# Performance work log

Measured on AMD Instinct MI355X. Metric: run time of the kernel, lower is better.

Reference implementation:

```python
import jax, jax.numpy as jnp
import numpy as np

P = 30          # points per cloud (nr_points)
K = 20          # knn neighbors (k)
KS = 5          # spline kernel size (control points)
FN = 10         # filter_nr
EPS = 1e-8


def setup_inputs() -> dict:
    key = jax.random.key(0)
    ks = jax.random.split(key, 7)
    B = 16384
    pos = jax.random.normal(ks[0], (B * P, 3), dtype=jnp.float32)
    W = jax.random.normal(ks[1], (KS, FN), dtype=jnp.float32) * 0.5
    b_dsc = jnp.zeros((FN,), dtype=jnp.float32)
    w1 = jax.random.normal(ks[2], (FN, 256), dtype=jnp.float32) * (1.0 / np.sqrt(FN))
    b1 = jnp.zeros((256,), dtype=jnp.float32)
    w2 = jax.random.normal(ks[3], (256, 40), dtype=jnp.float32) * (1.0 / np.sqrt(256.0))
    b2 = jnp.zeros((40,), dtype=jnp.float32)
    return {"pos": pos, "W": W, "b_dsc": b_dsc, "w1": w1, "b1": b1, "w2": w2, "b2": b2}


def _dsc(pos, W, b_dsc):
    # pos: [N,3] -> per-point directional spline conv features [N, FN]
    B = pos.shape[0] // P
    p = pos.reshape(B, P, 3)
    # knn within each cloud (loop=False): pairwise sq dists, mask self
    d2 = jnp.sum((p[:, :, None, :] - p[:, None, :, :]) ** 2, axis=-1)  # [B,P,P]
    d2 = d2 + jnp.eye(P, dtype=d2.dtype) * 1e10
    _, idx = jax.lax.top_k(-d2, K)  # [B,P,K] nearest neighbor indices
    nb = jax.vmap(lambda pts, ii: pts[ii])(p, idx)  # [B,P,K,3] gather
    rel = nb - p[:, :, None, :]                      # [B,P,K,3]
    # normalize neighborhood into unit ball
    norm = jnp.sqrt(jnp.sum(rel * rel, axis=-1) + EPS)      # [B,P,K]
    scale = jnp.max(norm, axis=-1, keepdims=True) + EPS     # [B,P,1]
    rel_n = rel / scale[..., None]
    # dominant local direction via power iteration on 3x3 covariance
    C = jnp.einsum('bpki,bpkj->bpij', rel_n, rel_n)  # [B,P,3,3]
    v = jnp.ones((B, P, 3), dtype=pos.dtype) / jnp.sqrt(3.0)
    for _ in range(8):
        v = jnp.einsum('bpij,bpj->bpi', C, v)
        v = v / (jnp.sqrt(jnp.sum(v * v, axis=-1, keepdims=True)) + EPS)
    # directional coordinate in [-1,1] -> spline parameter in [0, KS-1]
    t = jnp.einsum('bpki,bpi->bpk', rel_n, v)        # [B,P,K]
    u = jnp.clip((t + 1.0) * 0.5, 0.0, 1.0) * (KS - 1)
    i0 = jnp.clip(jnp.floor(u), 0, KS - 2).astype(jnp.int32)  # [B,P,K]
    frac = (u - i0.astype(u.dtype))[..., None]                 # [B,P,K,1]
    feat = W[i0] * (1.0 - frac) + W[i0 + 1] * frac             # [B,P,K,FN]
    y = jnp.mean(feat, axis=2) + b_dsc                         # [B,P,FN]
    return y.reshape(B * P, FN)


def reference(pos, W, b_dsc, w1, b1, w2, b2):
    y = _dsc(pos, W, b_dsc)                  # [N, FN]
    y = jax.nn.sigmoid(y)
    ys = y.reshape(-1, P, FN).mean(axis=1)   # [B, FN]
    h = jax.nn.elu(ys @ w1 + b1)             # [B, 256]
    logits = h @ w2 + b2                     # [B, 40]
    return jax.nn.log_softmax(logits, axis=1)
```

## Files before the change

kernel.cpp:

```cpp
#include <hip/hip_runtime.h>
#include <math.h>

#define NP 30
#define KNN 20
#define KS 5
#define FN 10
#define EPS 1e-8f
#define CPB 16
#define T1 512

typedef __attribute__((ext_vector_type(8))) short short8v;
typedef __attribute__((ext_vector_type(4))) float float4v;

__device__ __forceinline__ float satf(float x) {
    return fminf(fmaxf(x, 0.0f), 1.0f);
}
__device__ __forceinline__ unsigned short bf16r(float f) {
    unsigned u = __float_as_uint(f);
    u += 0x7fffu + ((u >> 16) & 1u);
    return (unsigned short)(u >> 16);
}
__device__ __forceinline__ float rlanef(float v, int l) {
    return __int_as_float(__builtin_amdgcn_readlane(__float_as_int(v), l));
}
__device__ __forceinline__ int hA_idx(int row, int col) {
    return row * 256 + ((((col >> 3) ^ (row & 7)) << 3) | (col & 7));
}
__device__ __forceinline__ float packdi(float v, int j) {
    return __uint_as_float((__float_as_uint(v) & ~31u) | (unsigned)j);
}

__global__ __launch_bounds__(T1, 4) void fused_kernel(
    const float* __restrict__ pos,
    const float* __restrict__ W,
    const float* __restrict__ b_dsc,
    const float* __restrict__ w1,
    const float* __restrict__ b1,
    const float* __restrict__ w2,
    const float* __restrict__ b2,
    float* __restrict__ out,
    int B)
{
    __shared__ float4 ptsF[CPB * NP];
    __shared__ float sb[CPB * NP][11];
    __shared__ __align__(16) float Gs[CPB][12];
    __shared__ float wS[KS * FN];
    __shared__ float bS[FN];
    __shared__ float ysS[CPB * FN];
    __shared__ __align__(16) unsigned short hA[16 * 256];
    __shared__ float Lg[CPB][48];

    const int tid  = threadIdx.x;
    const int base = blockIdx.x * CPB;
    const int w    = tid >> 6;
    const int lane = tid & 63;

    if (tid < CPB * NP) {
        int gp = base * NP + tid;
        if (gp < B * NP) {
            const float* pp = pos + (size_t)gp * 3;
            float x = pp[0], y = pp[1], z = pp[2];
            float n2 = fmaf(z, z, fmaf(y, y, x * x));
            ptsF[tid] = make_float4(x, y, z, n2);
        } else {
            ptsF[tid] = make_float4(0.f, 0.f, 0.f, 0.f);
        }
    }
    if (tid < KS * FN) wS[tid] = W[tid] * (-0.07213475204444817f);
    if (tid < FN)      bS[tid] = b_dsc[tid] * (-1.4426950408889634f);
    __syncthreads();

    const int c = tid / NP;
    const int i = tid - c * NP;
    const bool active = (tid < CPB * NP) && (base + c < B);

    float vals[32];
    float ox = 0.f, oy = 0.f, oz = 0.f, oo = 0.f;

    if (active) {
        const float4* cp = &ptsF[c * NP];
        float4 own = cp[i];
        ox = own.x; oy = own.y; oz = own.z; oo = own.w;

        sb[tid][0] = ox * ox; sb[tid][1] = ox * oy; sb[tid][2] = ox * oz;
        sb[tid][3] = oy * oy; sb[tid][4] = oy * oz; sb[tid][5] = oz * oz;
        sb[tid][6] = ox;      sb[tid][7] = oy;     sb[tid][8] = oz;

        #pragma unroll
        for (int j = 0; j < NP; ++j) {
            float4 q = cp[j];
            float dt = fmaf(q.z, oz, fmaf(q.y, oy, q.x * ox));
            float key = fmaf(-2.0f, dt, q.w);
            vals[j] = packdi(key, j);
            if ((j % 5) == 4) asm volatile("" ::: "memory");
        }
        vals[30] = packdi(1e11f, 30);
        vals[31] = packdi(1e11f, 31);

        #pragma unroll
        for (int k = 2; k <= 16; k <<= 1) {
            #pragma unroll
            for (int jj = k >> 1; jj > 0; jj >>= 1) {
                #pragma unroll
                for (int tt = 0; tt < 32; ++tt) {
                    int l = tt ^ jj;
                    if (l > tt) {
                        float a  = vals[tt], b = vals[l];
                        float lo = fminf(a, b), hi = fmaxf(a, b);
                        if ((tt & k) == 0) { vals[tt] = lo; vals[l] = hi; }
                        else               { vals[tt] = hi; vals[l] = lo; }
                    }
                }
            }
        }
        #pragma unroll
        for (int q = 0; q < 16; ++q) {
            float a = vals[q], b = vals[16 + q];
            vals[q] = fminf(a, b); vals[16 + q] = fmaxf(a, b);
        }
        #pragma unroll
        for (int jj = 8; jj > 0; jj >>= 1) {
            #pragma unroll
            for (int tt = 16; tt < 32; ++tt) {
                int l = tt ^ jj;
                if (l > tt) {
                    float a = vals[tt], b = vals[l];
                    vals[tt] = fminf(a, b); vals[l] = fmaxf(a, b);
                }
            }
        }
    }
    __syncthreads();

    if (tid < CPB * 9) {
        int cc   = tid / 9;
        int comp = tid - cc * 9;
        if (base + cc < B) {
            float s = 0.0f;
            #pragma unroll
            for (int k = 0; k < NP; ++k) s += sb[cc * NP + k][comp];
            Gs[cc][comp] = s;
        }
    }
    __syncthreads();

    if (active) {
        const float4* cp = &ptsF[c * NP];
        const float thr_key = __uint_as_float(__float_as_uint(vals[20]) & ~31u);
        const float thr_d2  = thr_key + oo;
        const float scale   = sqrtf(thr_d2 + EPS) + EPS;
        const float inv_s   = __builtin_amdgcn_rcpf(scale);

        float4 g0 = *(const float4*)&Gs[c][0];
        float4 g1 = *(const float4*)&Gs[c][4];
        float  sx = g1.z, sy = g1.w, sz = Gs[c][8];
        float ax = fmaf(30.f, ox, -sx);
        float ay = fmaf(30.f, oy, -sy);
        float az = fmaf(30.f, oz, -sz);
        float cxx = fmaf(ox, ax, fmaf(-sx, ox, g0.x));
        float cxy = fmaf(oy, ax, fmaf(-sy, ox, g0.y));
        float cxz = fmaf(oz, ax, fmaf(-sz, ox, g0.z));
        float cyy = fmaf(oy, ay, fmaf(-sy, oy, g0.w));
        float cyz = fmaf(oz, ay, fmaf(-sz, oy, g1.x));
        float czz = fmaf(oz, az, fmaf(-sz, oz, g1.y));

        unsigned excl = 0u;
        #pragma unroll
        for (int q2 = 21; q2 < 30; ++q2) {
            unsigned bq  = __float_as_uint(vals[q2]);
            int      idx = (int)(bq & 31u);
            float4 p = cp[idx];
            float dx = p.x - ox, dy = p.y - oy, dz = p.z - oz;
            cxx = fmaf(-dx, dx, cxx); cxy = fmaf(-dx, dy, cxy); cxz = fmaf(-dx, dz, cxz);
            cyy = fmaf(-dy, dy, cyy); cyz = fmaf(-dy, dz, cyz); czz = fmaf(-dz, dz, czz);
            excl |= (1u << idx);
        }

        float tr = cxx + cyy + czz + 1e-30f;
        float rt = __builtin_amdgcn_rcpf(tr);
        float xx = cxx*rt, xy = cxy*rt, xz = cxz*rt;
        float yy = cyy*rt, yz = cyz*rt, zz = czz*rt;
        #pragma unroll
        for (int it = 0; it < 3; ++it) {
            float nxx = fmaf(xx, xx, fmaf(xy, xy, xz * xz));
            float nxy = fmaf(xy, xx + yy, xz * yz);
            float nxz = fmaf(xz, xx + zz, xy * yz);
            float nyy = fmaf(xy, xy, fmaf(yy, yy, yz * yz));
            float nyz = fmaf(yz, yy + zz, xy * xz);
            float nzz = fmaf(xz, xz, fmaf(yz, yz, zz * zz));
            xx = nxx; xy = nxy; xz = nxz; yy = nyy; yz = nyz; zz = nzz;
        }
        float vx = xx + xy + xz;
        float vy = xy + yy + yz;
        float vz = xz + yz + zz;
        float nn = fmaf(vz, vz, fmaf(vy, vy, vx * vx)) + 1e-30f;
        float rr2 = __builtin_amdgcn_rsqf(nn) * inv_s * 2.0f;
        const float wax = vx * rr2, way = vy * rr2, waz = vz * rr2;
        const float c0  = 2.0f - fmaf(oz, waz, fmaf(oy, way, ox * wax));

        float a0 = 0.f, a1 = 0.f, a3 = 0.f, s1 = 0.f;
        #pragma unroll 5
        for (int j = 0; j < NP; ++j) {
            float4 q = cp[j];
            float ur = fmaf(q.z, waz, fmaf(q.y, way, fmaf(q.x, wax, c0)));
            float u  = ((excl >> j) & 1u) ? 2.0f : ur;
            a0 += satf(1.0f - u);
            a1 += satf(1.0f - fabsf(u - 1.0f));
            a3 += satf(1.0f - fabsf(u - 3.0f));
            s1 += u;
        }
        const float P  = 30.0f - a0 - a1 - a3;
        const float Q  = s1 - a1 - 3.0f * a3;
        const float a4 = fmaf(0.5f, Q, -P);
        const float a2 = P - a4 - 10.0f;

        #pragma unroll
        for (int f = 0; f < FN; ++f) {
            float acc = fmaf(a0, wS[0*FN+f],
                        fmaf(a1, wS[1*FN+f],
                        fmaf(a2, wS[2*FN+f],
                        fmaf(a3, wS[3*FN+f],
                             a4 * wS[4*FN+f]))));
            float z2 = acc + bS[f];
            sb[tid][f] = __builtin_amdgcn_rcpf(1.0f + exp2f(z2));
        }
    }
    __syncthreads();

    if (tid < CPB * FN) {
        int c2 = tid / FN;
        float s = 0.0f;
        #pragma unroll
        for (int jj = 0; jj < NP; ++jj) s += sb[c2 * NP + jj][tid - c2 * FN];
        ysS[tid] = (base + c2 < B) ? s * (1.0f / (float)NP) : 0.0f;
    }
    __syncthreads();

    {
        const int  hu    = tid & 255;
        const int  ybase = (w >= 4) ? 80 : 0;
        const int  rbase = (w >= 4) ? 8 : 0;
        float ya = ysS[ybase + lane];
        float yb = ysS[ybase + 64 + (lane & 15)];
        float wv[FN];
        #pragma unroll
        for (int f = 0; f < FN; ++f) wv[f] = w1[f * 256 + hu];
        float bb = b1[hu];
        #pragma unroll
        for (int cc = 0; cc < 8; ++cc) {
            float acc = bb;
            #pragma unroll
            for (int f = 0; f < FN; ++f) {
                const int flat = cc * FN + f;
                float yv = (flat < 64) ? rlanef(ya, flat) : rlanef(yb, flat - 64);
                acc = fmaf(yv, wv[f], acc);
            }
            float h = acc > 0.0f ? acc : __expf(acc) - 1.0f;
            hA[hA_idx(rbase + cc, hu)] = bf16r(h);
        }
    }
    __syncthreads();

    if (w < 3) {
        const int  n   = w * 16 + (lane & 15);
        const bool nok = n < 40;
        const int  kg  = (lane >> 4) * 8;
        float4v acc = {0.f, 0.f, 0.f, 0.f};
        #pragma unroll
        for (int s = 0; s < 8; ++s) {
            short8v bfr;
            #pragma unroll
            for (int j = 0; j < 8; ++j) {
                float f = nok ? w2[(s * 32 + kg + j) * 40 + n] : 0.0f;
                bfr[j] = (short)bf16r(f);
            }
            short8v a = *(const short8v*)&hA[hA_idx(lane & 15, kg + s * 32)];
            acc = __builtin_amdgcn_mfma_f32_16x16x32_bf16(a, bfr, acc, 0, 0, 0);
        }
        if (nok) {
            const float bc = b2[n];
            const int   r0 = (lane >> 4) * 4;
            #pragma unroll
            for (int r = 0; r < 4; ++r) {
                Lg[r0 + r][n] = acc[r] + bc;
            }
        }
    }
    __syncthreads();

    if (tid < CPB * 16) {
        int cl = tid >> 4, l = tid & 15;
        float v0 = Lg[cl][l];
        float v1 = Lg[cl][l + 16];
        float v2 = (l < 8) ? Lg[cl][l + 32] : -INFINITY;
        float m = fmaxf(fmaxf(v0, v1), v2);
        #pragma unroll
        for (int msk = 1; msk < 16; msk <<= 1) m = fmaxf(m, __shfl_xor(m, msk));
        float e = __expf(v0 - m) + __expf(v1 - m) + ((l < 8) ? __expf(v2 - m) : 0.0f);
        #pragma unroll
        for (int msk = 1; msk < 16; msk <<= 1) e += __shfl_xor(e, msk);
        float ls = m + __logf(e);
        int cloud = base + cl;
        if (cloud < B) {
            float* op = out + (size_t)cloud * 40;
            op[l]      = v0 - ls;
            op[16 + l] = v1 - ls;
            if (l < 8) op[32 + l] = v2 - ls;
        }
    }
}

extern "C" void kernel_launch(void* const* d_in, const int* in_sizes, int n_in,
                              void* d_out, int out_size, void* d_ws, size_t ws_size,
                              hipStream_t stream) {
    const float* pos   = (const float*)d_in[0];
    const float* W     = (const float*)d_in[1];
    const float* b_dsc = (const float*)d_in[2];
    const float* w1    = (const float*)d_in[3];
    const float* b1    = (const float*)d_in[4];
    const float* w2    = (const float*)d_in[5];
    const float* b2    = (const float*)d_in[6];

    const int N = in_sizes[0] / 3;
    const int B = N / NP;

    const int grid = (B + CPB - 1) / CPB;
    fused_kernel<<<grid, T1, 0, stream>>>(pos, W, b_dsc, w1, b1, w2, b2,
                                          (float*)d_out, B);
}
```

Measured before the change: 31.56 us.

## Replace full bitonic sort with pruned two-half selection network; read weights directly

```diff
diff --git a/kernel.cpp b/kernel.cpp
--- a/kernel.cpp
+++ b/kernel.cpp
@@ -29,6 +29,9 @@
 __device__ __forceinline__ float packdi(float v, int j) {
     return __uint_as_float((__float_as_uint(v) & ~31u) | (unsigned)j);
 }
+
+#define CEA(A, B) { float a_ = vals[A], b_ = vals[B]; vals[A] = fminf(a_, b_); vals[B] = fmaxf(a_, b_); }
+#define CED(A, B) { float a_ = vals[A], b_ = vals[B]; vals[A] = fmaxf(a_, b_); vals[B] = fminf(a_, b_); }
 
 __global__ __launch_bounds__(T1, 4) void fused_kernel(
     const float* __restrict__ pos,
@@ -44,8 +47,6 @@
     __shared__ float4 ptsF[CPB * NP];
     __shared__ float sb[CPB * NP][11];
     __shared__ __align__(16) float Gs[CPB][12];
-    __shared__ float wS[KS * FN];
-    __shared__ float bS[FN];
     __shared__ float ysS[CPB * FN];
     __shared__ __align__(16) unsigned short hA[16 * 256];
     __shared__ float Lg[CPB][48];
@@ -66,8 +67,6 @@
             ptsF[tid] = make_float4(0.f, 0.f, 0.f, 0.f);
         }
     }
-    if (tid < KS * FN) wS[tid] = W[tid] * (-0.07213475204444817f);
-    if (tid < FN)      bS[tid] = b_dsc[tid] * (-1.4426950408889634f);
     __syncthreads();
 
     const int c = tid / NP;
@@ -98,37 +97,30 @@
         vals[31] = packdi(1e11f, 31);
 
         #pragma unroll
-        for (int k = 2; k <= 16; k <<= 1) {
-            #pragma unroll
-            for (int jj = k >> 1; jj > 0; jj >>= 1) {
+        for (int p = 1; p < 16; p <<= 1) {
+            #pragma unroll
+            for (int k = p; k >= 1; k >>= 1) {
                 #pragma unroll
-                for (int tt = 0; tt < 32; ++tt) {
-                    int l = tt ^ jj;
-                    if (l > tt) {
-                        float a  = vals[tt], b = vals[l];
-                        float lo = fminf(a, b), hi = fmaxf(a, b);
-                        if ((tt & k) == 0) { vals[tt] = lo; vals[l] = hi; }
-                        else               { vals[tt] = hi; vals[l] = lo; }
+                for (int j = (k & (p - 1)); j + k < 16; j += 2 * k) {
+                    #pragma unroll
+                    for (int ii = 0; ii < k; ++ii) {
+                        if (ii + j + k < 16 &&
+                            ((ii + j) / (2 * p)) == ((ii + j + k) / (2 * p))) {
+                            CEA(ii + j, ii + j + k);
+                            CED(16 + ii + j, 16 + ii + j + k);
+                        }
                     }
                 }
             }
         }
         #pragma unroll
-        for (int q = 0; q < 16; ++q) {
-            float a = vals[q], b = vals[16 + q];
-            vals[q] = fminf(a, b); vals[16 + q] = fmaxf(a, b);
-        }
-        #pragma unroll
-        for (int jj = 8; jj > 0; jj >>= 1) {
-            #pragma unroll
-            for (int tt = 16; tt < 32; ++tt) {
-                int l = tt ^ jj;
-                if (l > tt) {
-                    float a = vals[tt], b = vals[l];
-                    vals[tt] = fminf(a, b); vals[l] = fmaxf(a, b);
-                }
-            }
-        }
+        for (int q = 0; q < 16; ++q) vals[16 + q] = fmaxf(vals[q], vals[16 + q]);
+        #pragma unroll
+        for (int q = 0; q < 8; ++q) { CEA(16 + q, 24 + q); }
+        CEA(16, 20) CEA(17, 21) CEA(18, 22) CEA(19, 23)
+        CEA(24, 28) CEA(25, 29) CEA(26, 30) CEA(27, 31)
+        CEA(20, 22) CEA(21, 23) CEA(24, 26) CEA(25, 27) CEA(28, 30) CEA(29, 31)
+        CEA(20, 21) CEA(22, 23) CEA(24, 25) CEA(26, 27) CEA(28, 29)
     }
     __syncthreads();
 
@@ -216,12 +208,13 @@
 
         #pragma unroll
         for (int f = 0; f < FN; ++f) {
-            float acc = fmaf(a0, wS[0*FN+f],
-                        fmaf(a1, wS[1*FN+f],
-                        fmaf(a2, wS[2*FN+f],
-                        fmaf(a3, wS[3*FN+f],
-                             a4 * wS[4*FN+f]))));
-            float z2 = acc + bS[f];
+            float acc = fmaf(a0, W[0*FN+f],
+                        fmaf(a1, W[1*FN+f],
+                        fmaf(a2, W[2*FN+f],
+                        fmaf(a3, W[3*FN+f],
+                             a4 * W[4*FN+f]))));
+            float bn = b_dsc[f] * (-1.4426950408889634f);
+            float z2 = fmaf(acc, -0.07213475204444817f, bn);
             sb[tid][f] = __builtin_amdgcn_rcpf(1.0f + exp2f(z2));
         }
     }
```

New measurement: 30.85 us. -2.2%, faster.
